# Kernel optimization log

Hardware: AMD Instinct MI355X
Metric: run time of the kernel (lower is better)

## Reference

```python
import jax, jax.numpy as jnp
import numpy as np

NC = 20          # num_classes
NA = 5           # num_anchors
NB = 64          # batch
NH = 38
NW = 38
MAXB = 50        # max GT boxes per image (hardcoded in build_targets)
COORD_SCALE = 1.0
NOOBJ = 1.0
OBJ = 5.0
CLS_SCALE = 1.0
THRESH = 0.6
ANCHORS = [1.3221, 1.73145, 3.19275, 4.00944, 5.05587, 8.09892, 9.47112, 4.84053, 11.2364, 10.0071]


def _iou_centered(b1, b2):
    """IoU for (cx,cy,w,h) boxes, broadcasting over leading dims. Matches bbox_ious(x1y1x2y2=False)."""
    mx = jnp.minimum(b1[..., 0] - b1[..., 2] * 0.5, b2[..., 0] - b2[..., 2] * 0.5)
    Mx = jnp.maximum(b1[..., 0] + b1[..., 2] * 0.5, b2[..., 0] + b2[..., 2] * 0.5)
    my = jnp.minimum(b1[..., 1] - b1[..., 3] * 0.5, b2[..., 1] - b2[..., 3] * 0.5)
    My = jnp.maximum(b1[..., 1] + b1[..., 3] * 0.5, b2[..., 1] + b2[..., 3] * 0.5)
    w1, h1, w2, h2 = b1[..., 2], b1[..., 3], b2[..., 2], b2[..., 3]
    cw = w1 + w2 - (Mx - mx)
    ch = h1 + h2 - (My - my)
    inter = jnp.where((cw <= 0) | (ch <= 0), 0.0, cw * ch)
    union = w1 * h1 + w2 * h2 - inter
    return inter / union


def setup_inputs() -> dict:
    key = jax.random.key(0)
    output = jax.random.normal(key, (NB, NA * (5 + NC), NH, NW), dtype=jnp.float32)
    # Structured GT: [cls, x, y, w, h] * 50 per image, zero-padded; distinct cells per image
    rng = np.random.default_rng(0)
    tgt = np.zeros((NB, MAXB * 5), np.float32)
    for b in range(NB):
        k = int(rng.integers(3, 16))
        cells = rng.choice(NH * NW, size=k, replace=False)
        gi = cells % NW
        gj = cells // NW
        tgt[b, 0:k * 5:5] = rng.integers(0, NC, k)
        tgt[b, 1:k * 5:5] = (gi + rng.uniform(0.2, 0.8, k)) / NW
        tgt[b, 2:k * 5:5] = (gj + rng.uniform(0.2, 0.8, k)) / NH
        tgt[b, 3:k * 5:5] = rng.uniform(0.05, 0.4, k)
        tgt[b, 4:k * 5:5] = rng.uniform(0.05, 0.4, k)
    return {"output": output, "target": jnp.asarray(tgt),
            "anchors": jnp.asarray(ANCHORS, dtype=jnp.float32)}


def _forward(output, target, anchors):
    nB, nA, nC, nH, nW = NB, NA, NC, NH, NW
    N = nB * nA * nH * nW
    sg = jax.lax.stop_gradient

    out = output.reshape(nB, nA, 5 + nC, nH, nW)
    x = jax.nn.sigmoid(out[:, :, 0])
    y = jax.nn.sigmoid(out[:, :, 1])
    w = out[:, :, 2]
    h = out[:, :, 3]
    conf = jax.nn.sigmoid(out[:, :, 4])
    # cls laid out flat in (b, a, h, w) order -> [N, nC]
    cls_flat = out[:, :, 5:].transpose(0, 1, 3, 4, 2).reshape(N, nC)

    aw = anchors.reshape(nA, 2)[:, 0]
    ah = anchors.reshape(nA, 2)[:, 1]

    # pred_boxes built from detached activations (x.data in torch)
    px = sg(x) + jnp.arange(nW, dtype=jnp.float32)[None, None, None, :]
    py = sg(y) + jnp.arange(nH, dtype=jnp.float32)[None, None, :, None]
    pw = jnp.exp(sg(w)) * sg(aw)[None, :, None, None]
    ph = jnp.exp(sg(h)) * sg(ah)[None, :, None, None]
    pred = jnp.stack([px, py, pw, ph], axis=-1).reshape(nB, nA * nH * nW, 4)

    # ---- build_targets (vectorized) ----
    tgt = sg(target).reshape(nB, MAXB, 5)
    valid = jnp.cumprod((tgt[:, :, 1] != 0).astype(jnp.float32), axis=1)  # break at first x==0
    gx = tgt[:, :, 1] * nW
    gy = tgt[:, :, 2] * nH
    gw = tgt[:, :, 3] * nW
    gh = tgt[:, :, 4] * nH
    gt = jnp.stack([gx, gy, gw, gh], axis=-1)  # [nB, MAXB, 4]

    # noobject suppression: max IoU of every pred box vs all valid GTs
    ious = _iou_centered(pred[:, :, None, :], gt[:, None, :, :]) * valid[:, None, :]
    max_iou = jnp.max(ious, axis=-1)  # [nB, nA*nH*nW]
    conf_mask = jnp.where(max_iou > THRESH, 0.0, NOOBJ).reshape(N)

    # seen < 12800 branch
    tx = jnp.full((N,), 0.5, jnp.float32)
    ty = jnp.full((N,), 0.5, jnp.float32)
    tw = jnp.zeros((N,), jnp.float32)
    th = jnp.zeros((N,), jnp.float32)
    coord_mask = jnp.ones((N,), jnp.float32)
    cls_mask = jnp.zeros((N,), jnp.float32)
    tconf = jnp.zeros((N,), jnp.float32)
    tcls = jnp.zeros((N,), jnp.float32)

    # best anchor per GT: origin-centered IoU anchor(0,0,aw,ah) vs gt(0,0,gw,gh)
    saw, sah = sg(aw), sg(ah)
    inter = jnp.minimum(saw[None, None, :], gw[:, :, None]) * jnp.minimum(sah[None, None, :], gh[:, :, None])
    union = saw[None, None, :] * sah[None, None, :] + (gw * gh)[:, :, None] - inter
    best_n = jnp.argmax(inter / union, axis=-1)  # [nB, MAXB]

    gi = jnp.clip(gx.astype(jnp.int32), 0, nW - 1)
    gj = jnp.clip(gy.astype(jnp.int32), 0, nH - 1)
    b_idx = jnp.broadcast_to(jnp.arange(nB)[:, None], (nB, MAXB))
    flat = ((b_idx * nA + best_n) * nH + gj) * nW + gi       # (b,a,h,w) flat order
    flat_sc = jnp.where(valid > 0, flat, N).reshape(-1)      # OOB index -> scatter dropped

    pred_flat = pred.reshape(N, 4)
    pb = pred_flat[jnp.clip(flat, 0, N - 1)]                 # matched pred box per GT
    iou_gt = _iou_centered(gt, pb)                           # [nB, MAXB]

    coord_mask = coord_mask.at[flat_sc].set(1.0)
    cls_mask = cls_mask.at[flat_sc].set(1.0)
    conf_mask = conf_mask.at[flat_sc].set(OBJ)
    tx = tx.at[flat_sc].set((gx - gi).reshape(-1))
    ty = ty.at[flat_sc].set((gy - gj).reshape(-1))
    tw = tw.at[flat_sc].set(jnp.log(gw / saw[best_n]).reshape(-1))
    th = th.at[flat_sc].set(jnp.log(gh / sah[best_n]).reshape(-1))
    tconf = tconf.at[flat_sc].set(iou_gt.reshape(-1))
    tcls = tcls.at[flat_sc].set(tgt[:, :, 0].reshape(-1))

    s4 = (nB, nA, nH, nW)
    cm = sg(coord_mask).reshape(s4)
    sm = jnp.sqrt(sg(conf_mask)).reshape(s4)
    clm = sg(cls_mask)

    loss_x = COORD_SCALE * jnp.sum((x * cm - sg(tx).reshape(s4) * cm) ** 2) / 2.0
    loss_y = COORD_SCALE * jnp.sum((y * cm - sg(ty).reshape(s4) * cm) ** 2) / 2.0
    loss_w = COORD_SCALE * jnp.sum((w * cm - sg(tw).reshape(s4) * cm) ** 2) / 2.0
    loss_h = COORD_SCALE * jnp.sum((h * cm - sg(th).reshape(s4) * cm) ** 2) / 2.0
    loss_conf = jnp.sum((conf * sm - sg(tconf).reshape(s4) * sm) ** 2) / 2.0

    logp = jax.nn.log_softmax(cls_flat, axis=-1)
    picked = jnp.take_along_axis(logp, sg(tcls).astype(jnp.int32)[:, None], axis=1)[:, 0]
    loss_cls = -CLS_SCALE * jnp.sum(picked * clm)

    return loss_x + loss_y + loss_w + loss_h + loss_conf + loss_cls


def reference(output, target, anchors):
    return _forward(output, target, anchors)
```

## Files before the change

kernel.cpp:

```cpp
#include <hip/hip_runtime.h>
#include <math.h>


#define NCc 20
#define NAc 5
#define NBc 64
#define NHc 38
#define NWc 38
#define MAXBc 50
#define NHWc (NHc * NWc)
#define CELLS_PER_B (NAc * NHWc)
#define BPB 29
#define THRESHc 0.6f
#define OBJc 5.0f

__global__ void zero_out_kernel(float* out) { out[0] = 0.0f; }

__global__ __launch_bounds__(256) void region_loss_kernel(
    const float* __restrict__ outp, const float* __restrict__ target,
    const float* __restrict__ anchors, float* __restrict__ loss_out)
{
    __shared__ float s_gx[MAXBc], s_gy[MAXBc], s_gw[MAXBc], s_gh[MAXBc];
    __shared__ float s_tx[MAXBc], s_ty[MAXBc], s_tw[MAXBc], s_th[MAXBc];
    __shared__ int   s_meta[MAXBc];
    __shared__ int   s_nvalid;
    __shared__ float s_aw[NAc], s_ah[NAc];
    __shared__ float s_red[4];

    const int tid  = threadIdx.x;
    const int b    = blockIdx.x / BPB;
    const int cell = (blockIdx.x % BPB) * 256 + tid;

    if (tid < NAc) {
        s_aw[tid] = anchors[2 * tid];
        s_ah[tid] = anchors[2 * tid + 1];
    }

    if (tid < 64) {
        const float* tb = target + (size_t)b * (MAXBc * 5);
        float gxn = (tid < MAXBc) ? tb[tid * 5 + 1] : 0.0f;
        unsigned long long m = __ballot(gxn != 0.0f);
        int nv = (int)__builtin_ctzll(~m);
        if (tid == 0) s_nvalid = nv;
        if (tid < nv) {
            float gx = gxn * (float)NWc;
            float gy = tb[tid * 5 + 2] * (float)NHc;
            float gw = tb[tid * 5 + 3] * (float)NWc;
            float gh = tb[tid * 5 + 4] * (float)NHc;
            int   cc = (int)tb[tid * 5 + 0];
            int bn = 0; float best = -1.0f;
            #pragma unroll
            for (int a = 0; a < NAc; ++a) {
                float aw = anchors[2 * a], ah = anchors[2 * a + 1];
                float inter = fminf(aw, gw) * fminf(ah, gh);
                float uni   = aw * ah + gw * gh - inter;
                float r = inter / uni;
                if (r > best) { best = r; bn = a; }
            }
            int gi = (int)gx; gi = min(max(gi, 0), NWc - 1);
            int gj = (int)gy; gj = min(max(gj, 0), NHc - 1);
            s_gx[tid] = gx; s_gy[tid] = gy; s_gw[tid] = gw; s_gh[tid] = gh;
            s_tx[tid] = gx - (float)gi;
            s_ty[tid] = gy - (float)gj;
            s_tw[tid] = __logf(gw / anchors[2 * bn]);
            s_th[tid] = __logf(gh / anchors[2 * bn + 1]);
            s_meta[tid] = bn | (gi << 3) | (gj << 9) | (cc << 15);
        }
    }
    __syncthreads();

    float lsum = 0.0f;
    if (cell < CELLS_PER_B) {
        const int a   = cell / NHWc;
        const int rem = cell - a * NHWc;
        const int j   = rem / NWc;
        const int i   = rem - j * NWc;

        const float* p = outp + ((size_t)(b * NAc + a) * (5 + NCc)) * NHWc + rem;
        float xr = p[0];
        float yr = p[NHWc];
        float wr = p[2 * NHWc];
        float hr = p[3 * NHWc];
        float cr = p[4 * NHWc];

        float x    = 1.0f / (1.0f + __expf(-xr));
        float y    = 1.0f / (1.0f + __expf(-yr));
        float conf = 1.0f / (1.0f + __expf(-cr));
        float pw = __expf(wr) * s_aw[a];
        float ph = __expf(hr) * s_ah[a];
        float px = x + (float)i;
        float py = y + (float)j;

        const int key = a | (i << 3) | (j << 9);
        float maxiou = 0.0f;
        float miou   = 0.0f;
        int   tmatch = -1;
        const int nv = s_nvalid;
        for (int t = 0; t < nv; ++t) {
            float gx = s_gx[t], gy = s_gy[t], gw = s_gw[t], gh = s_gh[t];
            float mx = fminf(px - pw * 0.5f, gx - gw * 0.5f);
            float Mx = fmaxf(px + pw * 0.5f, gx + gw * 0.5f);
            float my = fminf(py - ph * 0.5f, gy - gh * 0.5f);
            float My = fmaxf(py + ph * 0.5f, gy + gh * 0.5f);
            float cw = pw + gw - (Mx - mx);
            float chh = ph + gh - (My - my);
            float inter = (cw <= 0.0f || chh <= 0.0f) ? 0.0f : cw * chh;
            float uni = pw * ph + gw * gh - inter;
            float iou = inter / uni;
            maxiou = fmaxf(maxiou, iou);
            if ((s_meta[t] & 0x7FFF) == key) { tmatch = t; miou = iou; }
        }

        float tx, ty, tw, th, tc, cm;
        if (tmatch >= 0) {
            tx = s_tx[tmatch]; ty = s_ty[tmatch];
            tw = s_tw[tmatch]; th = s_th[tmatch];
            tc = miou; cm = OBJc;
        } else {
            tx = 0.5f; ty = 0.5f; tw = 0.0f; th = 0.0f; tc = 0.0f;
            cm = (maxiou > THRESHc) ? 0.0f : 1.0f;
        }
        float dx = x - tx, dy = y - ty, dw = wr - tw, dh = hr - th, dc = conf - tc;
        lsum = 0.5f * (dx * dx + dy * dy + dw * dw + dh * dh) + 0.5f * cm * dc * dc;

        if (tmatch >= 0) {
            int c = s_meta[tmatch] >> 15;
            const float* q = p + 5 * NHWc;
            float vals[NCc];
            float m = -1e30f, vc = 0.0f;
            #pragma unroll
            for (int k = 0; k < NCc; ++k) {
                vals[k] = q[k * NHWc];
                m = fmaxf(m, vals[k]);
                if (k == c) vc = vals[k];
            }
            float s = 0.0f;
            #pragma unroll
            for (int k = 0; k < NCc; ++k) s += __expf(vals[k] - m);
            lsum += (m + __logf(s)) - vc;
        }
    }

    float w = lsum;
    #pragma unroll
    for (int off = 32; off > 0; off >>= 1) w += __shfl_down(w, off, 64);
    if ((tid & 63) == 0) s_red[tid >> 6] = w;
    __syncthreads();
    if (tid == 0) {
        float tot = s_red[0] + s_red[1] + s_red[2] + s_red[3];
        atomicAdd(loss_out, tot);
    }
}

extern "C" void kernel_launch(void* const* d_in, const int* in_sizes, int n_in,
                              void* d_out, int out_size, void* d_ws, size_t ws_size,
                              hipStream_t stream) {
    const float* outp    = (const float*)d_in[0];
    const float* target  = (const float*)d_in[1];
    const float* anchors = (const float*)d_in[2];
    float* loss = (float*)d_out;

    zero_out_kernel<<<1, 1, 0, stream>>>(loss);
    region_loss_kernel<<<NBc * BPB, 256, 0, stream>>>(outp, target, anchors, loss);
}
```

Measured before the change: 105.2 us.

## Process four cells per thread with float4 loads and fewer blocks

```diff
diff --git a/kernel.cpp b/kernel.cpp
--- a/kernel.cpp
+++ b/kernel.cpp
@@ -10,11 +10,9 @@
 #define MAXBc 50
 #define NHWc (NHc * NWc)
 #define CELLS_PER_B (NAc * NHWc)
-#define BPB 29
+#define BPB 8
 #define THRESHc 0.6f
 #define OBJc 5.0f
-
-__global__ void zero_out_kernel(float* out) { out[0] = 0.0f; }
 
 __global__ __launch_bounds__(256) void region_loss_kernel(
     const float* __restrict__ outp, const float* __restrict__ target,
@@ -27,9 +25,9 @@
     __shared__ float s_aw[NAc], s_ah[NAc];
     __shared__ float s_red[4];
 
-    const int tid  = threadIdx.x;
-    const int b    = blockIdx.x / BPB;
-    const int cell = (blockIdx.x % BPB) * 256 + tid;
+    const int tid = threadIdx.x;
+    const int b   = blockIdx.x >> 3;
+    const int seg = blockIdx.x & 7;
 
     if (tid < NAc) {
         s_aw[tid] = anchors[2 * tid];
@@ -70,74 +68,94 @@
     __syncthreads();
 
     float lsum = 0.0f;
+    const int cell = seg * 1024 + tid * 4;
     if (cell < CELLS_PER_B) {
         const int a   = cell / NHWc;
         const int rem = cell - a * NHWc;
-        const int j   = rem / NWc;
-        const int i   = rem - j * NWc;
 
         const float* p = outp + ((size_t)(b * NAc + a) * (5 + NCc)) * NHWc + rem;
-        float xr = p[0];
-        float yr = p[NHWc];
-        float wr = p[2 * NHWc];
-        float hr = p[3 * NHWc];
-        float cr = p[4 * NHWc];
+        const float4 xr = *(const float4*)(p);
+        const float4 yr = *(const float4*)(p + NHWc);
+        const float4 wr = *(const float4*)(p + 2 * NHWc);
+        const float4 hr = *(const float4*)(p + 3 * NHWc);
+        const float4 cr = *(const float4*)(p + 4 * NHWc);
+        const float xrv[4] = {xr.x, xr.y, xr.z, xr.w};
+        const float yrv[4] = {yr.x, yr.y, yr.z, yr.w};
+        const float wrv[4] = {wr.x, wr.y, wr.z, wr.w};
+        const float hrv[4] = {hr.x, hr.y, hr.z, hr.w};
+        const float crv[4] = {cr.x, cr.y, cr.z, cr.w};
 
-        float x    = 1.0f / (1.0f + __expf(-xr));
-        float y    = 1.0f / (1.0f + __expf(-yr));
-        float conf = 1.0f / (1.0f + __expf(-cr));
-        float pw = __expf(wr) * s_aw[a];
-        float ph = __expf(hr) * s_ah[a];
-        float px = x + (float)i;
-        float py = y + (float)j;
+        float x[4], y[4], conf[4], pw[4], ph[4], px[4], py[4];
+        int key[4];
+        #pragma unroll
+        for (int k = 0; k < 4; ++k) {
+            const int rk = rem + k;
+            const int j  = rk / NWc;
+            const int i  = rk - j * NWc;
+            x[k]    = 1.0f / (1.0f + __expf(-xrv[k]));
+            y[k]    = 1.0f / (1.0f + __expf(-yrv[k]));
+            conf[k] = 1.0f / (1.0f + __expf(-crv[k]));
+            pw[k] = __expf(wrv[k]) * s_aw[a];
+            ph[k] = __expf(hrv[k]) * s_ah[a];
+            px[k] = x[k] + (float)i;
+            py[k] = y[k] + (float)j;
+            key[k] = a | (i << 3) | (j << 9);
+        }
 
-        const int key = a | (i << 3) | (j << 9);
-        float maxiou = 0.0f;
-        float miou   = 0.0f;
-        int   tmatch = -1;
+        float maxiou[4] = {0.0f, 0.0f, 0.0f, 0.0f};
+        float miou[4]   = {0.0f, 0.0f, 0.0f, 0.0f};
+        int   tmatch[4] = {-1, -1, -1, -1};
         const int nv = s_nvalid;
         for (int t = 0; t < nv; ++t) {
-            float gx = s_gx[t], gy = s_gy[t], gw = s_gw[t], gh = s_gh[t];
-            float mx = fminf(px - pw * 0.5f, gx - gw * 0.5f);
-            float Mx = fmaxf(px + pw * 0.5f, gx + gw * 0.5f);
-            float my = fminf(py - ph * 0.5f, gy - gh * 0.5f);
-            float My = fmaxf(py + ph * 0.5f, gy + gh * 0.5f);
-            float cw = pw + gw - (Mx - mx);
-            float chh = ph + gh - (My - my);
-            float inter = (cw <= 0.0f || chh <= 0.0f) ? 0.0f : cw * chh;
-            float uni = pw * ph + gw * gh - inter;
-            float iou = inter / uni;
-            maxiou = fmaxf(maxiou, iou);
-            if ((s_meta[t] & 0x7FFF) == key) { tmatch = t; miou = iou; }
+            const float gx = s_gx[t], gy = s_gy[t], gw = s_gw[t], gh = s_gh[t];
+            const int meta = s_meta[t] & 0x7FFF;
+            #pragma unroll
+            for (int k = 0; k < 4; ++k) {
+                float mx = fminf(px[k] - pw[k] * 0.5f, gx - gw * 0.5f);
+                float Mx = fmaxf(px[k] + pw[k] * 0.5f, gx + gw * 0.5f);
+                float my = fminf(py[k] - ph[k] * 0.5f, gy - gh * 0.5f);
+                float My = fmaxf(py[k] + ph[k] * 0.5f, gy + gh * 0.5f);
+                float cw  = pw[k] + gw - (Mx - mx);
+                float chh = ph[k] + gh - (My - my);
+                float inter = (cw <= 0.0f || chh <= 0.0f) ? 0.0f : cw * chh;
+                float uni = pw[k] * ph[k] + gw * gh - inter;
+                float iou = inter / uni;
+                maxiou[k] = fmaxf(maxiou[k], iou);
+                if (meta == key[k]) { tmatch[k] = t; miou[k] = iou; }
+            }
         }
 
-        float tx, ty, tw, th, tc, cm;
-        if (tmatch >= 0) {
-            tx = s_tx[tmatch]; ty = s_ty[tmatch];
-            tw = s_tw[tmatch]; th = s_th[tmatch];
-            tc = miou; cm = OBJc;
-        } else {
-            tx = 0.5f; ty = 0.5f; tw = 0.0f; th = 0.0f; tc = 0.0f;
-            cm = (maxiou > THRESHc) ? 0.0f : 1.0f;
-        }
-        float dx = x - tx, dy = y - ty, dw = wr - tw, dh = hr - th, dc = conf - tc;
-        lsum = 0.5f * (dx * dx + dy * dy + dw * dw + dh * dh) + 0.5f * cm * dc * dc;
+        #pragma unroll
+        for (int k = 0; k < 4; ++k) {
+            float tx, ty, tw, th, tc, cm;
+            if (tmatch[k] >= 0) {
+                tx = s_tx[tmatch[k]]; ty = s_ty[tmatch[k]];
+                tw = s_tw[tmatch[k]]; th = s_th[tmatch[k]];
+                tc = miou[k]; cm = OBJc;
+            } else {
+                tx = 0.5f; ty = 0.5f; tw = 0.0f; th = 0.0f; tc = 0.0f;
+                cm = (maxiou[k] > THRESHc) ? 0.0f : 1.0f;
+            }
+            float dx = x[k] - tx, dy = y[k] - ty;
+            float dw = wrv[k] - tw, dh = hrv[k] - th, dc = conf[k] - tc;
+            lsum += 0.5f * (dx * dx + dy * dy + dw * dw + dh * dh) + 0.5f * cm * dc * dc;
 
-        if (tmatch >= 0) {
-            int c = s_meta[tmatch] >> 15;
-            const float* q = p + 5 * NHWc;
-            float vals[NCc];
-            float m = -1e30f, vc = 0.0f;
-            #pragma unroll
-            for (int k = 0; k < NCc; ++k) {
-                vals[k] = q[k * NHWc];
-                m = fmaxf(m, vals[k]);
-                if (k == c) vc = vals[k];
+            if (tmatch[k] >= 0) {
+                int c = s_meta[tmatch[k]] >> 15;
+                const float* q = p + k + 5 * NHWc;
+                float vals[NCc];
+                float mm = -1e30f, vc = 0.0f;
+                #pragma unroll
+                for (int kk = 0; kk < NCc; ++kk) {
+                    vals[kk] = q[kk * NHWc];
+                    mm = fmaxf(mm, vals[kk]);
+                    if (kk == c) vc = vals[kk];
+                }
+                float s = 0.0f;
+                #pragma unroll
+                for (int kk = 0; kk < NCc; ++kk) s += __expf(vals[kk] - mm);
+                lsum += (mm + __logf(s)) - vc;
             }
-            float s = 0.0f;
-            #pragma unroll
-            for (int k = 0; k < NCc; ++k) s += __expf(vals[k] - m);
-            lsum += (m + __logf(s)) - vc;
         }
     }
 
@@ -160,6 +178,6 @@
     const float* anchors = (const float*)d_in[2];
     float* loss = (float*)d_out;
 
-    zero_out_kernel<<<1, 1, 0, stream>>>(loss);
+    hipMemsetAsync(loss, 0, sizeof(float), stream);
     region_loss_kernel<<<NBc * BPB, 256, 0, stream>>>(outp, target, anchors, loss);
 }
```

After: 94.23 us. 1.12x faster.
